# Optimization experiments

Hardware: AMD Instinct MI355X
Metric: run time of the kernel (lower is better)

The kernel has to match this reference:

```python
import jax, jax.numpy as jnp
import numpy as np

B, N, F_IN = 32, 512, 64
HEADS = (8, 8)
HIDS = (64, 64)
EDGE_P = 0.05  # graph density
NEG_SLOPE = 0.2
NEG_INF = -1e20


def setup_inputs() -> dict:
    key = jax.random.key(0)
    ks = jax.random.split(key, 8)
    x = jax.random.normal(ks[0], (B, N, F_IN), dtype=jnp.float32)
    adj = (jax.random.uniform(ks[1], (B, N, N)) < EDGE_P).astype(jnp.float32)
    adj = jnp.maximum(adj, adj.transpose(0, 2, 1))  # symmetric adjacency
    # mask = (batch, row): every (b, n) pair gets the masked softmax
    b_idx = jnp.repeat(jnp.arange(B, dtype=jnp.int32), N)   # [B*N]
    r_idx = jnp.tile(jnp.arange(N, dtype=jnp.int32), B)     # [B*N]
    # layer 0: f_in=64 -> f_out=64, H=8 ; layer 1: f_in=64*8=512 -> f_out=64, H=8
    W0 = jax.random.normal(ks[2], (F_IN, HIDS[0]), dtype=jnp.float32) / jnp.sqrt(jnp.float32(F_IN))
    a_src0 = jax.random.normal(ks[3], (HIDS[0], HEADS[0]), dtype=jnp.float32) / jnp.sqrt(jnp.float32(HIDS[0]))
    a_dst0 = jax.random.normal(ks[4], (HIDS[0], HEADS[0]), dtype=jnp.float32) / jnp.sqrt(jnp.float32(HIDS[0]))
    f_in1 = HIDS[0] * HEADS[0]
    W1 = jax.random.normal(ks[5], (f_in1, HIDS[1]), dtype=jnp.float32) / jnp.sqrt(jnp.float32(f_in1))
    a_src1 = jax.random.normal(ks[6], (HIDS[1], HEADS[1]), dtype=jnp.float32) / jnp.sqrt(jnp.float32(HIDS[1]))
    a_dst1 = jax.random.normal(ks[7], (HIDS[1], HEADS[1]), dtype=jnp.float32) / jnp.sqrt(jnp.float32(HIDS[1]))
    return dict(x=x, adj=adj, b_idx=b_idx, r_idx=r_idx,
                W0=W0, a_src0=a_src0, a_dst0=a_dst0,
                W1=W1, a_src1=a_src1, a_dst1=a_dst1)


def _gat_layer(x, adj, b_idx, r_idx, W, a_src, a_dst):
    # x: [B,N,f_in], adj: [B,N,N] (diag already set), W: [f_in,F], a_*: [F,H]
    hp = x @ W                                        # [B,N,F]
    s = jnp.einsum('bnf,fh->bhn', hp, a_src)          # attn_src
    d = jnp.einsum('bnf,fh->bhn', hp, a_dst)          # attn_dst
    attn = s[:, :, :, None] + d[:, :, None, :]        # [B,H,N,N]
    attn = jnp.where(attn >= 0, attn, NEG_SLOPE * attn)  # leaky_relu(0.2)
    attn = jnp.where(adj[:, None, :, :] == 0, 0.0, attn)  # masked_fill(adj==0, 0)
    rows = attn[b_idx, :, r_idx, :]                   # [K,H,N]
    rows = jnp.where(rows == 0.0, NEG_INF, rows)
    rows = jax.nn.softmax(rows, axis=-1)
    attn = attn.at[b_idx, :, r_idx, :].set(rows)
    return jnp.einsum('bhij,bjf->bhif', attn, hp)     # [B,H,N,F]


def reference(x, adj, b_idx, r_idx, W0, a_src0, a_dst0, W1, a_src1, a_dst1):
    Bn, Nn = x.shape[:2]
    # torch mutates adj in place: adj[batch,row,row] = 1 (self loops)
    adj = adj.at[b_idx, r_idx, r_idx].set(1.0)
    o = _gat_layer(x, adj, b_idx, r_idx, W0, a_src0, a_dst0)      # [B,H,N,F0]
    x1 = jax.nn.elu(o.transpose(0, 2, 1, 3).reshape(Bn, Nn, -1))  # [B,N,H*F0]
    o2 = _gat_layer(x1, adj, b_idx, r_idx, W1, a_src1, a_dst1)    # [B,H,N,F1]
    return o2.mean(axis=1)                                        # [B,N,F1]
```

## Files before the change

### kernel.cpp

```cpp
#include <hip/hip_runtime.h>
#include <hip/hip_bf16.h>
#include <math.h>

#define BB 32
#define NN 512

typedef short bf16x8 __attribute__((ext_vector_type(8)));
typedef float f32x4 __attribute__((ext_vector_type(4)));

static __device__ __forceinline__ unsigned short f2bf(float v) {
    __hip_bfloat16 h = __float2bfloat16(v);
    return __builtin_bit_cast(unsigned short, h);
}
static __device__ __forceinline__ float bf2f(unsigned short u) {
    __hip_bfloat16 h = __builtin_bit_cast(__hip_bfloat16, u);
    return __bfloat162float(h);
}

__global__ __launch_bounds__(256) void k_wt_prep(
    const float* __restrict__ W, int KT,
    unsigned short* __restrict__ Wh, unsigned short* __restrict__ Wl)
{
    int id = blockIdx.x * 256 + threadIdx.x;
    int n = id & 63, gabs = id >> 6;
    if (gabs >= (KT >> 3)) return;
    int c = gabs >> 3, gl = gabs & 7;
    int p = gl ^ (n & 7);
    bf16x8 hv, lv;
#pragma unroll
    for (int e = 0; e < 8; ++e) {
        float v = W[(size_t)(gabs * 8 + e) * 64 + n];
        unsigned short hb = f2bf(v);
        hv[e] = (short)hb;
        lv[e] = (short)f2bf(v - bf2f(hb));
    }
    size_t g = (size_t)n * KT + c * 64 + p * 8;
    *(bf16x8*)(Wh + g) = hv;
    *(bf16x8*)(Wl + g) = lv;
}

static __device__ __forceinline__ void epi_sd_hpt(
    const float* ctile, const float* asd_f, int row0, int t,
    float* __restrict__ s, float* __restrict__ d,
    unsigned short* __restrict__ hpTh, unsigned short* __restrict__ hpTl)
{
    if (t < 128) {
        int rr = t >> 3, h = t & 7;
        float sv = 0.f, dv = 0.f;
#pragma unroll
        for (int f = 0; f < 64; ++f) {
            float hv = ctile[rr * 66 + f];
            sv = fmaf(hv, asd_f[f * 8 + h], sv);
            dv = fmaf(hv, asd_f[512 + f * 8 + h], dv);
        }
        s[(size_t)(row0 + rr) * 8 + h] = sv;
        d[(size_t)(row0 + rr) * 8 + h] = dv;
    } else {
        int t2 = t - 128;
        int f = t2 >> 1, jl = (t2 & 1) * 8;
        bf16x8 hv, lv;
#pragma unroll
        for (int e = 0; e < 8; ++e) {
            float v = ctile[(jl + e) * 66 + f];
            unsigned short hb = f2bf(v);
            hv[e] = (short)hb;
            lv[e] = (short)f2bf(v - bf2f(hb));
        }
        int b = row0 >> 9, jb = row0 & 511;
        int jj = jb + jl;
        int cch = jj >> 6, p = ((jj >> 3) & 7) ^ (f & 7);
        size_t g = ((size_t)b * 64 + f) * 512 + cch * 64 + p * 8;
        *(bf16x8*)(hpTh + g) = hv;
        *(bf16x8*)(hpTl + g) = lv;
    }
}

__global__ __launch_bounds__(256) void k_gemm0(
    const float* __restrict__ x,
    const unsigned short* __restrict__ W0Th, const unsigned short* __restrict__ W0Tl,
    const float* __restrict__ a_src, const float* __restrict__ a_dst,
    float* __restrict__ s, float* __restrict__ d,
    unsigned short* __restrict__ hpTh, unsigned short* __restrict__ hpTl)
{
    __shared__ short Ah[16 * 64], Al[16 * 64];
    __shared__ short Bh[64 * 64], Bl[64 * 64];
    __shared__ float ctile[16 * 66];
    __shared__ float asd_f[1024];

    int t = threadIdx.x;
    int row0 = blockIdx.x * 16;

    ((float4*)asd_f)[t] = (t < 128) ? ((const float4*)a_src)[t]
                                    : ((const float4*)a_dst)[t - 128];
    {
        int n = t >> 2, gp = (t & 3) * 2;
#pragma unroll
        for (int u = 0; u < 2; ++u) {
            *(uint4*)&Bh[n * 64 + (gp + u) * 8] = *(const uint4*)(W0Th + (size_t)n * 64 + (gp + u) * 8);
            *(uint4*)&Bl[n * 64 + (gp + u) * 8] = *(const uint4*)(W0Tl + (size_t)n * 64 + (gp + u) * 8);
        }
    }
    if (t < 128) {
        int row = t >> 3, g = t & 7;
        const float4* src = (const float4*)(x + (size_t)(row0 + row) * 64 + g * 8);
        float4 v0 = src[0], v1 = src[1];
        float vv[8] = {v0.x, v0.y, v0.z, v0.w, v1.x, v1.y, v1.z, v1.w};
        bf16x8 hv, lv;
#pragma unroll
        for (int e = 0; e < 8; ++e) {
            unsigned short hb = f2bf(vv[e]);
            hv[e] = (short)hb;
            lv[e] = (short)f2bf(vv[e] - bf2f(hb));
        }
        int p = g ^ (row & 7);
        *(bf16x8*)&Ah[row * 64 + p * 8] = hv;
        *(bf16x8*)&Al[row * 64 + p * 8] = lv;
    }
    __syncthreads();

    int lane = t & 63, w = t >> 6, cn = lane & 15, rq = lane >> 4;
    f32x4 acc, acc2;
#pragma unroll
    for (int e = 0; e < 4; ++e) { acc[e] = 0.f; acc2[e] = 0.f; }

#pragma unroll
    for (int ks = 0; ks < 2; ++ks) {
        int pa = ((ks * 4 + rq) ^ (cn & 7)) * 8;
        bf16x8 ah = *(const bf16x8*)&Ah[cn * 64 + pa];
        bf16x8 al = *(const bf16x8*)&Al[cn * 64 + pa];
        int nn = w * 16 + cn;
        int pb = ((ks * 4 + rq) ^ (cn & 7)) * 8;
        bf16x8 bh = *(const bf16x8*)&Bh[nn * 64 + pb];
        bf16x8 bl = *(const bf16x8*)&Bl[nn * 64 + pb];
        acc  = __builtin_amdgcn_mfma_f32_16x16x32_bf16(ah, bh, acc, 0, 0, 0);
        acc2 = __builtin_amdgcn_mfma_f32_16x16x32_bf16(ah, bl, acc2, 0, 0, 0);
        acc2 = __builtin_amdgcn_mfma_f32_16x16x32_bf16(al, bh, acc2, 0, 0, 0);
    }
#pragma unroll
    for (int r = 0; r < 4; ++r)
        ctile[(rq * 4 + r) * 66 + w * 16 + cn] = acc[r] + acc2[r];
    __syncthreads();
    epi_sd_hpt(ctile, asd_f, row0, t, s, d, hpTh, hpTl);
}

__global__ __launch_bounds__(256) void k_gemm1(
    const unsigned short* __restrict__ x1h, const unsigned short* __restrict__ x1l,
    const unsigned short* __restrict__ W1Th, const unsigned short* __restrict__ W1Tl,
    const float* __restrict__ a_src, const float* __restrict__ a_dst,
    float* __restrict__ s, float* __restrict__ d,
    unsigned short* __restrict__ hpTh, unsigned short* __restrict__ hpTl)
{
    __shared__ short Ah[16 * 64], Al[16 * 64];
    __shared__ short Bh[64 * 64], Bl[64 * 64];
    __shared__ float ctile[16 * 66];
    __shared__ float asd_f[1024];

    int t = threadIdx.x;
    int row0 = blockIdx.x * 16;
    ((float4*)asd_f)[t] = (t < 128) ? ((const float4*)a_src)[t]
                                    : ((const float4*)a_dst)[t - 128];

    int ar = (t & 127) >> 3, ag = t & 7;
    const unsigned short* asrc = (t < 128) ? x1h : x1l;
    short* adst = (t < 128) ? Ah : Al;
    int bn = t >> 2, bg0 = (t & 3) * 2;

    uint4 ra, rb0, rb1, rb2, rb3;
    ra  = *(const uint4*)(asrc + (size_t)(row0 + ar) * 512 + ag * 8);
    rb0 = *(const uint4*)(W1Th + (size_t)bn * 512 + (bg0 + 0) * 8);
    rb1 = *(const uint4*)(W1Th + (size_t)bn * 512 + (bg0 + 1) * 8);
    rb2 = *(const uint4*)(W1Tl + (size_t)bn * 512 + (bg0 + 0) * 8);
    rb3 = *(const uint4*)(W1Tl + (size_t)bn * 512 + (bg0 + 1) * 8);

    int lane = t & 63, w = t >> 6, cn = lane & 15, rq = lane >> 4;
    f32x4 acc, acc2;
#pragma unroll
    for (int e = 0; e < 4; ++e) { acc[e] = 0.f; acc2[e] = 0.f; }

    for (int kc = 0; kc < 8; ++kc) {
        *(uint4*)&adst[ar * 64 + ag * 8] = ra;
        *(uint4*)&Bh[bn * 64 + (bg0 + 0) * 8] = rb0;
        *(uint4*)&Bh[bn * 64 + (bg0 + 1) * 8] = rb1;
        *(uint4*)&Bl[bn * 64 + (bg0 + 0) * 8] = rb2;
        *(uint4*)&Bl[bn * 64 + (bg0 + 1) * 8] = rb3;
        __syncthreads();
        if (kc < 7) {
            int k0 = (kc + 1) * 64;
            ra  = *(const uint4*)(asrc + (size_t)(row0 + ar) * 512 + k0 + ag * 8);
            rb0 = *(const uint4*)(W1Th + (size_t)bn * 512 + k0 + (bg0 + 0) * 8);
            rb1 = *(const uint4*)(W1Th + (size_t)bn * 512 + k0 + (bg0 + 1) * 8);
            rb2 = *(const uint4*)(W1Tl + (size_t)bn * 512 + k0 + (bg0 + 0) * 8);
            rb3 = *(const uint4*)(W1Tl + (size_t)bn * 512 + k0 + (bg0 + 1) * 8);
        }
#pragma unroll
        for (int ks = 0; ks < 2; ++ks) {
            int pa = ((ks * 4 + rq) ^ (cn & 7)) * 8;
            bf16x8 ah = *(const bf16x8*)&Ah[cn * 64 + pa];
            bf16x8 al = *(const bf16x8*)&Al[cn * 64 + pa];
            int nn = w * 16 + cn;
            bf16x8 bh = *(const bf16x8*)&Bh[nn * 64 + pa];
            bf16x8 bl = *(const bf16x8*)&Bl[nn * 64 + pa];
            acc  = __builtin_amdgcn_mfma_f32_16x16x32_bf16(ah, bh, acc, 0, 0, 0);
            acc2 = __builtin_amdgcn_mfma_f32_16x16x32_bf16(ah, bl, acc2, 0, 0, 0);
            acc2 = __builtin_amdgcn_mfma_f32_16x16x32_bf16(al, bh, acc2, 0, 0, 0);
        }
        __syncthreads();
    }
#pragma unroll
    for (int r = 0; r < 4; ++r)
        ctile[(rq * 4 + r) * 66 + w * 16 + cn] = acc[r] + acc2[r];
    __syncthreads();
    epi_sd_hpt(ctile, asd_f, row0, t, s, d, hpTh, hpTl);
}

__global__ __launch_bounds__(256, 4) void k_attn_mfma(
    const float* __restrict__ adj, const float* __restrict__ s,
    const float* __restrict__ d,
    const unsigned short* __restrict__ hpTh,
    const unsigned short* __restrict__ hpTl,
    unsigned short* __restrict__ o_h, unsigned short* __restrict__ o_l,
    float* __restrict__ o_f, int mode)
{
    __shared__ short hT[2][8192];
    __shared__ float dT[2][8 * 68];
    __shared__ unsigned long long maskL[2][16];
    __shared__ float inv[128];
    float* red = (float*)&hT[0][0];

    int blk = blockIdx.x;
    int vb = ((blk & 7) << 7) | (blk >> 3);
    int b = vb >> 5, i0 = (vb & 31) << 4;
    int t = threadIdx.x, lane = t & 63, w = t >> 6;
    int cn = lane & 15, rq = lane >> 4;
    int h0 = w * 2, h1 = h0 + 1;

    float sv0 = s[((size_t)b * NN + i0 + cn) * 8 + h0];
    float sv1 = s[((size_t)b * NN + i0 + cn) * 8 + h1];

    const float* adjb = adj + ((size_t)b * NN + i0) * NN;
    const unsigned short* hbh = hpTh + (size_t)b * 64 * 512;
    const unsigned short* hbl = hpTl + (size_t)b * 64 * 512;

#pragma unroll
    for (int pp = 0; pp < 4; ++pp) {
        int row = pp * 4 + w;
        float a = adjb[(size_t)row * NN + lane];
        bool bit = (a != 0.f) || ((i0 + row) == lane);
        unsigned long long m = __ballot(bit);
        if (lane == 0) maskL[0][row] = m;
    }
    if (t < 128) {
        int j = t >> 1, h4 = (t & 1) * 4;
        float4 dv = *(const float4*)(d + ((size_t)b * NN + j) * 8 + h4);
        dT[0][(h4 + 0) * 68 + j] = dv.x;
        dT[0][(h4 + 1) * 68 + j] = dv.y;
        dT[0][(h4 + 2) * 68 + j] = dv.z;
        dT[0][(h4 + 3) * 68 + j] = dv.w;
    }
#pragma unroll
    for (int u = 0; u < 2; ++u) {
        int idx = t + u * 256;
        int f = idx >> 3, g = idx & 7;
        *(uint4*)&hT[0][f * 64 + g * 8]        = *(const uint4*)(hbh + (size_t)f * 512 + g * 8);
        *(uint4*)&hT[0][4096 + f * 64 + g * 8] = *(const uint4*)(hbl + (size_t)f * 512 + g * 8);
    }
    __syncthreads();

    f32x4 acc[2][4];
#pragma unroll
    for (int hh = 0; hh < 2; ++hh)
#pragma unroll
        for (int ft = 0; ft < 4; ++ft)
#pragma unroll
            for (int e = 0; e < 4; ++e) acc[hh][ft][e] = 0.f;
    float rs0 = 0.f, rs1 = 0.f;

    for (int jcx = 0; jcx < 8; ++jcx) {
        int cur = jcx & 1, nxt = cur ^ 1;
        int jcn = (jcx + 1) * 64;
        bool pf = jcx < 7;
        float pa[4];
        float4 pd;
        uint4 ph0, ph1, pl0, pl1;
        if (pf) {
#pragma unroll
            for (int pp = 0; pp < 4; ++pp)
                pa[pp] = adjb[(size_t)(pp * 4 + w) * NN + jcn + lane];
            if (t < 128) {
                int j = t >> 1, h4 = (t & 1) * 4;
                pd = *(const float4*)(d + ((size_t)b * NN + jcn + j) * 8 + h4);
            }
            {
                int f0 = t >> 3, g0 = t & 7;
                int f1 = (t + 256) >> 3, g1 = t & 7;
                ph0 = *(const uint4*)(hbh + (size_t)f0 * 512 + jcn + g0 * 8);
                pl0 = *(const uint4*)(hbl + (size_t)f0 * 512 + jcn + g0 * 8);
                ph1 = *(const uint4*)(hbh + (size_t)f1 * 512 + jcn + g1 * 8);
                pl1 = *(const uint4*)(hbl + (size_t)f1 * 512 + jcn + g1 * 8);
            }
        }

        unsigned long long mk = maskL[cur][cn];
        bf16x8 aA[2], aB[2];
#pragma unroll
        for (int ks = 0; ks < 2; ++ks) {
            int shift = ks * 32 + rq * 8;
            unsigned int mb = (unsigned int)(mk >> shift) & 0xffu;
            const float* dp0 = &dT[cur][h0 * 68 + shift];
            const float* dp1 = &dT[cur][h1 * 68 + shift];
            float4 da0 = *(const float4*)dp0, da1 = *(const float4*)(dp0 + 4);
            float4 db0 = *(const float4*)dp1, db1 = *(const float4*)(dp1 + 4);
            float dd0[8] = {da0.x, da0.y, da0.z, da0.w, da1.x, da1.y, da1.z, da1.w};
            float dd1[8] = {db0.x, db0.y, db0.z, db0.w, db1.x, db1.y, db1.z, db1.w};
#pragma unroll
            for (int e = 0; e < 8; ++e) {
                bool mbit = (mb >> e) & 1;
                float e0 = sv0 + dd0[e];
                e0 = fmaxf(e0, 0.2f * e0);
                float p0 = (mbit && e0 != 0.f) ? __expf(e0) : 0.f;
                rs0 += p0;
                float e1 = sv1 + dd1[e];
                e1 = fmaxf(e1, 0.2f * e1);
                float p1 = (mbit && e1 != 0.f) ? __expf(e1) : 0.f;
                rs1 += p1;
                aA[ks][e] = (short)f2bf(p0);
                aB[ks][e] = (short)f2bf(p1);
            }
        }
#pragma unroll
        for (int ks = 0; ks < 2; ++ks)
#pragma unroll
            for (int ft = 0; ft < 4; ++ft) {
                int f = ft * 16 + cn;
                int pb = ((ks * 4 + rq) ^ (f & 7)) * 8;
                bf16x8 bh = *(const bf16x8*)&hT[cur][f * 64 + pb];
                bf16x8 bl = *(const bf16x8*)&hT[cur][4096 + f * 64 + pb];
                acc[0][ft] = __builtin_amdgcn_mfma_f32_16x16x32_bf16(aA[ks], bh, acc[0][ft], 0, 0, 0);
                acc[0][ft] = __builtin_amdgcn_mfma_f32_16x16x32_bf16(aA[ks], bl, acc[0][ft], 0, 0, 0);
                acc[1][ft] = __builtin_amdgcn_mfma_f32_16x16x32_bf16(aB[ks], bh, acc[1][ft], 0, 0, 0);
                acc[1][ft] = __builtin_amdgcn_mfma_f32_16x16x32_bf16(aB[ks], bl, acc[1][ft], 0, 0, 0);
            }

        if (pf) {
#pragma unroll
            for (int pp = 0; pp < 4; ++pp) {
                int row = pp * 4 + w;
                bool bit = (pa[pp] != 0.f) || ((i0 + row) == (jcn + lane));
                unsigned long long m = __ballot(bit);
                if (lane == 0) maskL[nxt][row] = m;
            }
            if (t < 128) {
                int j = t >> 1, h4 = (t & 1) * 4;
                dT[nxt][(h4 + 0) * 68 + j] = pd.x;
                dT[nxt][(h4 + 1) * 68 + j] = pd.y;
                dT[nxt][(h4 + 2) * 68 + j] = pd.z;
                dT[nxt][(h4 + 3) * 68 + j] = pd.w;
            }
            {
                int f0 = t >> 3, g0 = t & 7;
                int f1 = (t + 256) >> 3;
                *(uint4*)&hT[nxt][f0 * 64 + g0 * 8]        = ph0;
                *(uint4*)&hT[nxt][4096 + f0 * 64 + g0 * 8] = pl0;
                *(uint4*)&hT[nxt][f1 * 64 + g0 * 8]        = ph1;
                *(uint4*)&hT[nxt][4096 + f1 * 64 + g0 * 8] = pl1;
            }
        }
        __syncthreads();
    }

    rs0 += __shfl_xor(rs0, 16); rs0 += __shfl_xor(rs0, 32);
    rs1 += __shfl_xor(rs1, 16); rs1 += __shfl_xor(rs1, 32);
    if (rq == 0) {
        inv[h0 * 16 + cn] = 1.0f / rs0;
        inv[h1 * 16 + cn] = 1.0f / rs1;
    }
    __syncthreads();

    if (mode == 0) {
#pragma unroll
        for (int hh = 0; hh < 2; ++hh) {
            int h = h0 + hh;
#pragma unroll
            for (int ft = 0; ft < 4; ++ft)
#pragma unroll
                for (int r = 0; r < 4; ++r) {
                    int il = rq * 4 + r;
                    float v = acc[hh][ft][r] * inv[h * 16 + il];
                    v = v > 0.f ? v : __expf(v) - 1.f;
                    int g = ft * 2 + (cn >> 3);
                    int p = g ^ (il & 7);
                    size_t addr = ((size_t)b * NN + i0 + il) * 512 + h * 64 + p * 8 + (cn & 7);
                    unsigned short hb = f2bf(v);
                    o_h[addr] = hb;
                    o_l[addr] = f2bf(v - bf2f(hb));
                }
        }
    } else {
#pragma unroll
        for (int ft = 0; ft < 4; ++ft)
#pragma unroll
            for (int r = 0; r < 4; ++r) {
                int il = rq * 4 + r;
                float v = acc[0][ft][r] * inv[h0 * 16 + il]
                        + acc[1][ft][r] * inv[h1 * 16 + il];
                red[(w * 16 + il) * 64 + ft * 16 + cn] = v;
            }
        __syncthreads();
#pragma unroll
        for (int u = 0; u < 4; ++u) {
            int idx = t + u * 256;
            int il = idx >> 6, f = idx & 63;
            float sum = red[il * 64 + f] + red[(16 + il) * 64 + f]
                      + red[(32 + il) * 64 + f] + red[(48 + il) * 64 + f];
            o_f[((size_t)b * NN + i0 + il) * 64 + f] = sum * 0.125f;
        }
    }
}

extern "C" void kernel_launch(void* const* d_in, const int* in_sizes, int n_in,
                              void* d_out, int out_size, void* d_ws, size_t ws_size,
                              hipStream_t stream) {
    const float* x      = (const float*)d_in[0];
    const float* adj    = (const float*)d_in[1];
    const float* W0     = (const float*)d_in[4];
    const float* a_src0 = (const float*)d_in[5];
    const float* a_dst0 = (const float*)d_in[6];
    const float* W1     = (const float*)d_in[7];
    const float* a_src1 = (const float*)d_in[8];
    const float* a_dst1 = (const float*)d_in[9];
    float* out = (float*)d_out;

    float* ws = (float*)d_ws;
    const size_t R = (size_t)BB * NN;
    float* s0 = ws;
    float* d0 = s0 + R * 8;
    float* s1 = d0 + R * 8;
    float* d1 = s1 + R * 8;
    unsigned short* x1h  = (unsigned short*)(d1 + R * 8);
    unsigned short* x1l  = x1h + R * 512;
    unsigned short* hp0h = x1l + R * 512;
    unsigned short* hp0l = hp0h + (size_t)BB * 64 * NN;
    unsigned short* hp1h = hp0l + (size_t)BB * 64 * NN;
    unsigned short* hp1l = hp1h + (size_t)BB * 64 * NN;
    unsigned short* W0Th = hp1l + (size_t)BB * 64 * NN;
    unsigned short* W0Tl = W0Th + (size_t)64 * 64;
    unsigned short* W1Th = W0Tl + (size_t)64 * 64;
    unsigned short* W1Tl = W1Th + (size_t)64 * 512;

    k_wt_prep<<<2, 256, 0, stream>>>(W0, 64, W0Th, W0Tl);
    k_wt_prep<<<16, 256, 0, stream>>>(W1, 512, W1Th, W1Tl);
    k_gemm0<<<1024, 256, 0, stream>>>(x, W0Th, W0Tl, a_src0, a_dst0, s0, d0, hp0h, hp0l);
    k_attn_mfma<<<1024, 256, 0, stream>>>(adj, s0, d0, hp0h, hp0l, x1h, x1l, nullptr, 0);
    k_gemm1<<<1024, 256, 0, stream>>>(x1h, x1l, W1Th, W1Tl, a_src1, a_dst1, s1, d1, hp1h, hp1l);
    k_attn_mfma<<<1024, 256, 0, stream>>>(adj, s1, d1, hp1h, hp1l, nullptr, nullptr, out, 1);
}
```

Measured before the change: 190.8 us.

## Fuse layer-1 GEMM into layer-0 attention epilogue and compute row sums via MFMA

The layer-0 attention kernel now runs the x1 @ W1 GEMM and the s/d/hp epilogue itself. It stages its ELU output tile in shared memory, so the x1 hi/lo intermediate no longer round-trips through global memory and one launch is removed. Softmax row sums now come from an MFMA against a ones vector instead of scalar adds and shuffles, the two weight-prep launches are merged into one, and a redundant index computation is dropped. The cost is more MFMA work, extra shared-memory reuse, and reloading the W1 tiles in every attention block.

Measured after the change: 192.1 us. Within noise of the previous version (+0.7%).

```diff
diff --git a/kernel.cpp b/kernel.cpp
--- a/kernel.cpp
+++ b/kernel.cpp
@@ -18,12 +18,14 @@
 }
 
 __global__ __launch_bounds__(256) void k_wt_prep(
-    const float* __restrict__ W, int KT,
-    unsigned short* __restrict__ Wh, unsigned short* __restrict__ Wl)
+    const float* __restrict__ W0, unsigned short* __restrict__ W0h, unsigned short* __restrict__ W0l,
+    const float* __restrict__ W1, unsigned short* __restrict__ W1h, unsigned short* __restrict__ W1l)
 {
     int id = blockIdx.x * 256 + threadIdx.x;
-    int n = id & 63, gabs = id >> 6;
-    if (gabs >= (KT >> 3)) return;
+    const float* W; unsigned short *Wh, *Wl; int KT, task;
+    if (id < 512) { W = W0; Wh = W0h; Wl = W0l; KT = 64;  task = id; }
+    else          { W = W1; Wh = W1h; Wl = W1l; KT = 512; task = id - 512; }
+    int n = task & 63, gabs = task >> 6;
     int c = gabs >> 3, gl = gabs & 7;
     int p = gl ^ (n & 7);
     bf16x8 hv, lv;
@@ -129,9 +131,8 @@
         bf16x8 ah = *(const bf16x8*)&Ah[cn * 64 + pa];
         bf16x8 al = *(const bf16x8*)&Al[cn * 64 + pa];
         int nn = w * 16 + cn;
-        int pb = ((ks * 4 + rq) ^ (cn & 7)) * 8;
-        bf16x8 bh = *(const bf16x8*)&Bh[nn * 64 + pb];
-        bf16x8 bl = *(const bf16x8*)&Bl[nn * 64 + pb];
+        bf16x8 bh = *(const bf16x8*)&Bh[nn * 64 + pa];
+        bf16x8 bl = *(const bf16x8*)&Bl[nn * 64 + pa];
         acc  = __builtin_amdgcn_mfma_f32_16x16x32_bf16(ah, bh, acc, 0, 0, 0);
         acc2 = __builtin_amdgcn_mfma_f32_16x16x32_bf16(ah, bl, acc2, 0, 0, 0);
         acc2 = __builtin_amdgcn_mfma_f32_16x16x32_bf16(al, bh, acc2, 0, 0, 0);
@@ -143,93 +144,25 @@
     epi_sd_hpt(ctile, asd_f, row0, t, s, d, hpTh, hpTl);
 }
 
-__global__ __launch_bounds__(256) void k_gemm1(
-    const unsigned short* __restrict__ x1h, const unsigned short* __restrict__ x1l,
+template<int MODE>
+__global__ __launch_bounds__(256, 4) void k_attn_fused(
+    const float* __restrict__ adj, const float* __restrict__ s,
+    const float* __restrict__ d,
+    const unsigned short* __restrict__ hpTh, const unsigned short* __restrict__ hpTl,
     const unsigned short* __restrict__ W1Th, const unsigned short* __restrict__ W1Tl,
     const float* __restrict__ a_src, const float* __restrict__ a_dst,
-    float* __restrict__ s, float* __restrict__ d,
-    unsigned short* __restrict__ hpTh, unsigned short* __restrict__ hpTl)
+    float* __restrict__ s_out, float* __restrict__ d_out,
+    unsigned short* __restrict__ hpOh, unsigned short* __restrict__ hpOl,
+    float* __restrict__ o_f)
 {
-    __shared__ short Ah[16 * 64], Al[16 * 64];
-    __shared__ short Bh[64 * 64], Bl[64 * 64];
-    __shared__ float ctile[16 * 66];
-    __shared__ float asd_f[1024];
-
-    int t = threadIdx.x;
-    int row0 = blockIdx.x * 16;
-    ((float4*)asd_f)[t] = (t < 128) ? ((const float4*)a_src)[t]
-                                    : ((const float4*)a_dst)[t - 128];
-
-    int ar = (t & 127) >> 3, ag = t & 7;
-    const unsigned short* asrc = (t < 128) ? x1h : x1l;
-    short* adst = (t < 128) ? Ah : Al;
-    int bn = t >> 2, bg0 = (t & 3) * 2;
-
-    uint4 ra, rb0, rb1, rb2, rb3;
-    ra  = *(const uint4*)(asrc + (size_t)(row0 + ar) * 512 + ag * 8);
-    rb0 = *(const uint4*)(W1Th + (size_t)bn * 512 + (bg0 + 0) * 8);
-    rb1 = *(const uint4*)(W1Th + (size_t)bn * 512 + (bg0 + 1) * 8);
-    rb2 = *(const uint4*)(W1Tl + (size_t)bn * 512 + (bg0 + 0) * 8);
-    rb3 = *(const uint4*)(W1Tl + (size_t)bn * 512 + (bg0 + 1) * 8);
-
-    int lane = t & 63, w = t >> 6, cn = lane & 15, rq = lane >> 4;
-    f32x4 acc, acc2;
-#pragma unroll
-    for (int e = 0; e < 4; ++e) { acc[e] = 0.f; acc2[e] = 0.f; }
-
-    for (int kc = 0; kc < 8; ++kc) {
-        *(uint4*)&adst[ar * 64 + ag * 8] = ra;
-        *(uint4*)&Bh[bn * 64 + (bg0 + 0) * 8] = rb0;
-        *(uint4*)&Bh[bn * 64 + (bg0 + 1) * 8] = rb1;
-        *(uint4*)&Bl[bn * 64 + (bg0 + 0) * 8] = rb2;
-        *(uint4*)&Bl[bn * 64 + (bg0 + 1) * 8] = rb3;
-        __syncthreads();
-        if (kc < 7) {
-            int k0 = (kc + 1) * 64;
-            ra  = *(const uint4*)(asrc + (size_t)(row0 + ar) * 512 + k0 + ag * 8);
-            rb0 = *(const uint4*)(W1Th + (size_t)bn * 512 + k0 + (bg0 + 0) * 8);
-            rb1 = *(const uint4*)(W1Th + (size_t)bn * 512 + k0 + (bg0 + 1) * 8);
-            rb2 = *(const uint4*)(W1Tl + (size_t)bn * 512 + k0 + (bg0 + 0) * 8);
-            rb3 = *(const uint4*)(W1Tl + (size_t)bn * 512 + k0 + (bg0 + 1) * 8);
-        }
-#pragma unroll
-        for (int ks = 0; ks < 2; ++ks) {
-            int pa = ((ks * 4 + rq) ^ (cn & 7)) * 8;
-            bf16x8 ah = *(const bf16x8*)&Ah[cn * 64 + pa];
-            bf16x8 al = *(const bf16x8*)&Al[cn * 64 + pa];
-            int nn = w * 16 + cn;
-            bf16x8 bh = *(const bf16x8*)&Bh[nn * 64 + pa];
-            bf16x8 bl = *(const bf16x8*)&Bl[nn * 64 + pa];
-            acc  = __builtin_amdgcn_mfma_f32_16x16x32_bf16(ah, bh, acc, 0, 0, 0);
-            acc2 = __builtin_amdgcn_mfma_f32_16x16x32_bf16(ah, bl, acc2, 0, 0, 0);
-            acc2 = __builtin_amdgcn_mfma_f32_16x16x32_bf16(al, bh, acc2, 0, 0, 0);
-        }
-        __syncthreads();
-    }
-#pragma unroll
-    for (int r = 0; r < 4; ++r)
-        ctile[(rq * 4 + r) * 66 + w * 16 + cn] = acc[r] + acc2[r];
-    __syncthreads();
-    epi_sd_hpt(ctile, asd_f, row0, t, s, d, hpTh, hpTl);
-}
-
-__global__ __launch_bounds__(256, 4) void k_attn_mfma(
-    const float* __restrict__ adj, const float* __restrict__ s,
-    const float* __restrict__ d,
-    const unsigned short* __restrict__ hpTh,
-    const unsigned short* __restrict__ hpTl,
-    unsigned short* __restrict__ o_h, unsigned short* __restrict__ o_l,
-    float* __restrict__ o_f, int mode)
-{
-    __shared__ short hT[2][8192];
-    __shared__ float dT[2][8 * 68];
+    __shared__ __align__(16) short hT[2][8192];
+    __shared__ __align__(16) float dTbuf[1088];
     __shared__ unsigned long long maskL[2][16];
-    __shared__ float inv[128];
-    float* red = (float*)&hT[0][0];
 
     int blk = blockIdx.x;
     int vb = ((blk & 7) << 7) | (blk >> 3);
     int b = vb >> 5, i0 = (vb & 31) << 4;
+    int row0 = vb * 16;
     int t = threadIdx.x, lane = t & 63, w = t >> 6;
     int cn = lane & 15, rq = lane >> 4;
     int h0 = w * 2, h1 = h0 + 1;
@@ -240,6 +173,10 @@
     const float* adjb = adj + ((size_t)b * NN + i0) * NN;
     const unsigned short* hbh = hpTh + (size_t)b * 64 * 512;
     const unsigned short* hbl = hpTl + (size_t)b * 64 * 512;
+
+    bf16x8 onesv;
+#pragma unroll
+    for (int e = 0; e < 8; ++e) onesv[e] = (short)0x3F80;
 
 #pragma unroll
     for (int pp = 0; pp < 4; ++pp) {
@@ -252,10 +189,10 @@
     if (t < 128) {
         int j = t >> 1, h4 = (t & 1) * 4;
         float4 dv = *(const float4*)(d + ((size_t)b * NN + j) * 8 + h4);
-        dT[0][(h4 + 0) * 68 + j] = dv.x;
-        dT[0][(h4 + 1) * 68 + j] = dv.y;
-        dT[0][(h4 + 2) * 68 + j] = dv.z;
-        dT[0][(h4 + 3) * 68 + j] = dv.w;
+        dTbuf[(h4 + 0) * 68 + j] = dv.x;
+        dTbuf[(h4 + 1) * 68 + j] = dv.y;
+        dTbuf[(h4 + 2) * 68 + j] = dv.z;
+        dTbuf[(h4 + 3) * 68 + j] = dv.w;
     }
 #pragma unroll
     for (int u = 0; u < 2; ++u) {
@@ -266,14 +203,16 @@
     }
     __syncthreads();
 
-    f32x4 acc[2][4];
-#pragma unroll
-    for (int hh = 0; hh < 2; ++hh)
+    f32x4 acc[2][4], accrs[2];
+#pragma unroll
+    for (int hh = 0; hh < 2; ++hh) {
+#pragma unroll
+        for (int e = 0; e < 4; ++e) accrs[hh][e] = 0.f;
 #pragma unroll
         for (int ft = 0; ft < 4; ++ft)
 #pragma unroll
             for (int e = 0; e < 4; ++e) acc[hh][ft][e] = 0.f;
-    float rs0 = 0.f, rs1 = 0.f;
+    }
 
     for (int jcx = 0; jcx < 8; ++jcx) {
         int cur = jcx & 1, nxt = cur ^ 1;
@@ -292,11 +231,11 @@
             }
             {
                 int f0 = t >> 3, g0 = t & 7;
-                int f1 = (t + 256) >> 3, g1 = t & 7;
+                int f1 = (t + 256) >> 3;
                 ph0 = *(const uint4*)(hbh + (size_t)f0 * 512 + jcn + g0 * 8);
                 pl0 = *(const uint4*)(hbl + (size_t)f0 * 512 + jcn + g0 * 8);
-                ph1 = *(const uint4*)(hbh + (size_t)f1 * 512 + jcn + g1 * 8);
-                pl1 = *(const uint4*)(hbl + (size_t)f1 * 512 + jcn + g1 * 8);
+                ph1 = *(const uint4*)(hbh + (size_t)f1 * 512 + jcn + g0 * 8);
+                pl1 = *(const uint4*)(hbl + (size_t)f1 * 512 + jcn + g0 * 8);
             }
         }
 
@@ -306,8 +245,8 @@
         for (int ks = 0; ks < 2; ++ks) {
             int shift = ks * 32 + rq * 8;
             unsigned int mb = (unsigned int)(mk >> shift) & 0xffu;
-            const float* dp0 = &dT[cur][h0 * 68 + shift];
-            const float* dp1 = &dT[cur][h1 * 68 + shift];
+            const float* dp0 = &dTbuf[cur * 544 + h0 * 68 + shift];
+            const float* dp1 = &dTbuf[cur * 544 + h1 * 68 + shift];
             float4 da0 = *(const float4*)dp0, da1 = *(const float4*)(dp0 + 4);
             float4 db0 = *(const float4*)dp1, db1 = *(const float4*)(dp1 + 4);
             float dd0[8] = {da0.x, da0.y, da0.z, da0.w, da1.x, da1.y, da1.z, da1.w};
@@ -318,17 +257,17 @@
                 float e0 = sv0 + dd0[e];
                 e0 = fmaxf(e0, 0.2f * e0);
                 float p0 = (mbit && e0 != 0.f) ? __expf(e0) : 0.f;
-                rs0 += p0;
                 float e1 = sv1 + dd1[e];
                 e1 = fmaxf(e1, 0.2f * e1);
                 float p1 = (mbit && e1 != 0.f) ? __expf(e1) : 0.f;
-                rs1 += p1;
                 aA[ks][e] = (short)f2bf(p0);
                 aB[ks][e] = (short)f2bf(p1);
             }
         }
 #pragma unroll
-        for (int ks = 0; ks < 2; ++ks)
+        for (int ks = 0; ks < 2; ++ks) {
+            accrs[0] = __builtin_amdgcn_mfma_f32_16x16x32_bf16(aA[ks], onesv, accrs[0], 0, 0, 0);
+            accrs[1] = __builtin_amdgcn_mfma_f32_16x16x32_bf16(aB[ks], onesv, accrs[1], 0, 0, 0);
 #pragma unroll
             for (int ft = 0; ft < 4; ++ft) {
                 int f = ft * 16 + cn;
@@ -340,6 +279,7 @@
                 acc[1][ft] = __builtin_amdgcn_mfma_f32_16x16x32_bf16(aB[ks], bh, acc[1][ft], 0, 0, 0);
                 acc[1][ft] = __builtin_amdgcn_mfma_f32_16x16x32_bf16(aB[ks], bl, acc[1][ft], 0, 0, 0);
             }
+        }
 
         if (pf) {
 #pragma unroll
@@ -351,10 +291,10 @@
             }
             if (t < 128) {
                 int j = t >> 1, h4 = (t & 1) * 4;
-                dT[nxt][(h4 + 0) * 68 + j] = pd.x;
-                dT[nxt][(h4 + 1) * 68 + j] = pd.y;
-                dT[nxt][(h4 + 2) * 68 + j] = pd.z;
-                dT[nxt][(h4 + 3) * 68 + j] = pd.w;
+                dTbuf[nxt * 544 + (h4 + 0) * 68 + j] = pd.x;
+                dTbuf[nxt * 544 + (h4 + 1) * 68 + j] = pd.y;
+                dTbuf[nxt * 544 + (h4 + 2) * 68 + j] = pd.z;
+                dTbuf[nxt * 544 + (h4 + 3) * 68 + j] = pd.w;
             }
             {
                 int f0 = t >> 3, g0 = t & 7;
@@ -368,41 +308,78 @@
         __syncthreads();
     }
 
-    rs0 += __shfl_xor(rs0, 16); rs0 += __shfl_xor(rs0, 32);
-    rs1 += __shfl_xor(rs1, 16); rs1 += __shfl_xor(rs1, 32);
-    if (rq == 0) {
-        inv[h0 * 16 + cn] = 1.0f / rs0;
-        inv[h1 * 16 + cn] = 1.0f / rs1;
-    }
-    __syncthreads();
-
-    if (mode == 0) {
-#pragma unroll
-        for (int hh = 0; hh < 2; ++hh) {
-            int h = h0 + hh;
-#pragma unroll
-            for (int ft = 0; ft < 4; ++ft)
-#pragma unroll
-                for (int r = 0; r < 4; ++r) {
-                    int il = rq * 4 + r;
-                    float v = acc[hh][ft][r] * inv[h * 16 + il];
-                    v = v > 0.f ? v : __expf(v) - 1.f;
-                    int g = ft * 2 + (cn >> 3);
-                    int p = g ^ (il & 7);
-                    size_t addr = ((size_t)b * NN + i0 + il) * 512 + h * 64 + p * 8 + (cn & 7);
-                    unsigned short hb = f2bf(v);
-                    o_h[addr] = hb;
-                    o_l[addr] = f2bf(v - bf2f(hb));
-                }
-        }
+    float invr[2][4];
+#pragma unroll
+    for (int hh = 0; hh < 2; ++hh)
+#pragma unroll
+        for (int r = 0; r < 4; ++r) invr[hh][r] = 1.0f / accrs[hh][r];
+
+    if (MODE == 0) {
+        ((float4*)dTbuf)[t] = (t < 128) ? ((const float4*)a_src)[t]
+                                        : ((const float4*)a_dst)[t - 128];
+        short* Bh   = &hT[0][0];
+        short* Bl   = &hT[1][0];
+        short* x1hc = &hT[0][4096];
+        short* x1lc = &hT[0][6144];
+        f32x4 g1, g2;
+#pragma unroll
+        for (int e = 0; e < 4; ++e) { g1[e] = 0.f; g2[e] = 0.f; }
+
+        for (int kc = 0; kc < 8; ++kc) {
+#pragma unroll
+            for (int u = 0; u < 2; ++u) {
+                int g = t + u * 256;
+                size_t src = (size_t)(g >> 3) * 512 + kc * 64 + (g & 7) * 8;
+                *(uint4*)&Bh[g * 8] = *(const uint4*)(W1Th + src);
+                *(uint4*)&Bl[g * 8] = *(const uint4*)(W1Tl + src);
+            }
+            if (w == (kc >> 1)) {
+                int hh = kc & 1;
+#pragma unroll
+                for (int ft = 0; ft < 4; ++ft)
+#pragma unroll
+                    for (int r = 0; r < 4; ++r) {
+                        int il = rq * 4 + r;
+                        float v = acc[hh][ft][r] * invr[hh][r];
+                        v = v > 0.f ? v : __expf(v) - 1.f;
+                        unsigned short hb = f2bf(v);
+                        float lo = v - bf2f(hb);
+                        int f = ft * 16 + cn;
+                        int addr = il * 64 + ((f >> 3) ^ (il & 7)) * 8 + (f & 7);
+                        x1hc[addr] = (short)hb;
+                        x1lc[addr] = (short)f2bf(lo);
+                    }
+            }
+            __syncthreads();
+#pragma unroll
+            for (int ks = 0; ks < 2; ++ks) {
+                int pa = ((ks * 4 + rq) ^ (cn & 7)) * 8;
+                bf16x8 ah = *(const bf16x8*)&x1hc[cn * 64 + pa];
+                bf16x8 al = *(const bf16x8*)&x1lc[cn * 64 + pa];
+                int nn = w * 16 + cn;
+                bf16x8 bh = *(const bf16x8*)&Bh[nn * 64 + pa];
+                bf16x8 bl = *(const bf16x8*)&Bl[nn * 64 + pa];
+                g1 = __builtin_amdgcn_mfma_f32_16x16x32_bf16(ah, bh, g1, 0, 0, 0);
+                g2 = __builtin_amdgcn_mfma_f32_16x16x32_bf16(ah, bl, g2, 0, 0, 0);
+                g2 = __builtin_amdgcn_mfma_f32_16x16x32_bf16(al, bh, g2, 0, 0, 0);
+            }
+            __syncthreads();
+        }
+        float* ctile = (float*)&hT[1][4096];
+#pragma unroll
+        for (int r = 0; r < 4; ++r)
+            ctile[(rq * 4 + r) * 66 + w * 16 + cn] = g1[r] + g2[r];
+        __syncthreads();
+        epi_sd_hpt(ctile, dTbuf, row0, t, s_out, d_out, hpOh, hpOl);
     } else {
+        float* red = (float*)&hT[0][0];
 #pragma unroll
         for (int ft = 0; ft < 4; ++ft)
 #pragma unroll
             for (int r = 0; r < 4; ++r) {
                 int il = rq * 4 + r;
-                float v = acc[0][ft][r] * inv[h0 * 16 + il]
-                        + acc[1][ft][r] * inv[h1 * 16 + il];
+                float v = acc[0][ft][r] * invr[0][r]
+                        + acc[1][ft][r] * invr[1][r];
                 red[(w * 16 + il) * 64 + ft * 16 + cn] = v;
             }
         __syncthreads();
@@ -436,9 +413,7 @@
     float* d0 = s0 + R * 8;
     float* s1 = d0 + R * 8;
     float* d1 = s1 + R * 8;
-    unsigned short* x1h  = (unsigned short*)(d1 + R * 8);
-    unsigned short* x1l  = x1h + R * 512;
-    unsigned short* hp0h = x1l + R * 512;
+    unsigned short* hp0h = (unsigned short*)(d1 + R * 8);
     unsigned short* hp0l = hp0h + (size_t)BB * 64 * NN;
     unsigned short* hp1h = hp0l + (size_t)BB * 64 * NN;
     unsigned short* hp1l = hp1h + (size_t)BB * 64 * NN;
@@ -447,10 +422,12 @@
     unsigned short* W1Th = W0Tl + (size_t)64 * 64;
     unsigned short* W1Tl = W1Th + (size_t)64 * 512;
 
-    k_wt_prep<<<2, 256, 0, stream>>>(W0, 64, W0Th, W0Tl);
-    k_wt_prep<<<16, 256, 0, stream>>>(W1, 512, W1Th, W1Tl);
+    k_wt_prep<<<18, 256, 0, stream>>>(W0, W0Th, W0Tl, W1, W1Th, W1Tl);
     k_gemm0<<<1024, 256, 0, stream>>>(x, W0Th, W0Tl, a_src0, a_dst0, s0, d0, hp0h, hp0l);
-    k_attn_mfma<<<1024, 256, 0, stream>>>(adj, s0, d0, hp0h, hp0l, x1h, x1l, nullptr, 0);
-    k_gemm1<<<1024, 256, 0, stream>>>(x1h, x1l, W1Th, W1Tl, a_src1, a_dst1, s1, d1, hp1h, hp1l);
-    k_attn_mfma<<<1024, 256, 0, stream>>>(adj, s1, d1, hp1h, hp1l, nullptr, nullptr, out, 1);
-}
+    k_attn_fused<0><<<1024, 256, 0, stream>>>(adj, s0, d0, hp0h, hp0l,
+                                              W1Th, W1Tl, a_src1, a_dst1,
+                                              s1, d1, hp1h, hp1l, nullptr);
+    k_attn_fused<1><<<1024, 256, 0, stream>>>(adj, s1, d1, hp1h, hp1l,
+                                              nullptr, nullptr, nullptr, nullptr,
+                                              nullptr, nullptr, nullptr, nullptr, out);
+}
```
